# Kernel optimization log

Measured on AMD Instinct MI355X. Metric: run time of the kernel, lower is better.

Reference implementation:

```python
import jax, jax.numpy as jnp
import numpy as np

N_NODES = 100000


def gcn_conv(x, W, b, src, dst, n):
    # PyG GCNConv: add self-loops, symmetric deg^-1/2 normalization,
    # transform then gather/scatter-add aggregate.
    loop = jnp.arange(n, dtype=src.dtype)
    s = jnp.concatenate([src, loop])
    d = jnp.concatenate([dst, loop])
    deg = jax.ops.segment_sum(jnp.ones_like(d, dtype=x.dtype), d, num_segments=n)
    dinv = jnp.where(deg > 0, 1.0 / jnp.sqrt(deg), 0.0)
    norm = dinv[s] * dinv[d]                      # [E+N]
    h = x @ W                                     # [N, out]
    msgs = h[s] * norm[:, None]                   # gather + scale
    out = jax.ops.segment_sum(msgs, d, num_segments=n)  # scatter-add
    return out + b


def setup_inputs() -> dict:
    key = jax.random.key(0)
    k1, k2, k3, k4 = jax.random.split(key, 4)
    F_in, H, D = 128, 16, 128
    x = jax.random.normal(k1, (N_NODES, F_in), dtype=jnp.float32)
    edge_index = jax.random.randint(k2, (2, 1600000), 0, N_NODES, dtype=jnp.int64)
    W1 = jax.random.normal(k3, (F_in, H), dtype=jnp.float32) / np.sqrt(F_in)
    b1 = jnp.zeros((H,), dtype=jnp.float32)
    W2 = jax.random.normal(k4, (H, D), dtype=jnp.float32) / np.sqrt(H)
    b2 = jnp.zeros((D,), dtype=jnp.float32)
    return {"x": x, "edge_index": edge_index, "W1": W1, "b1": b1, "W2": W2, "b2": b2}


def reference(x, edge_index, W1, b1, W2, b2):
    src, dst = edge_index[0], edge_index[1]
    n = x.shape[0]
    h = jax.nn.relu(gcn_conv(x, W1, b1, src, dst, n))
    out = jax.nn.relu(gcn_conv(h, W2, b2, src, dst, n))
    return out
```

## Files before the change

### kernel.cpp

```cpp
#include <hip/hip_runtime.h>
#include <hip/hip_fp16.h>
#include <stdint.h>

#define F_IN  128
#define HID   16
#define F_OUT 128
#define NBK   512
#define NBLK  256
#define BCAP  4096

__device__ __forceinline__ int bucket_of(int d, int N) {
    return (int)(((long long)d * NBK) / N);
}
__device__ __forceinline__ int bucket_lo(int b, int N) {
    return (int)(((long long)b * N + NBK - 1) / NBK);
}

__global__ void k_partf(const int* __restrict__ ei, int* __restrict__ bcur,
                        uint32_t* __restrict__ pairs, int E, int N) {
    __shared__ int lh[NBK], lbase[NBK], lcur[NBK], lnlo[NBK];
    int blk = blockIdx.x, t = threadIdx.x;
    int C = (E + NBLK - 1) / NBLK;
    int e0 = blk * C;
    int e1 = e0 + C; if (e1 > E) e1 = E;
    for (int i = t; i < NBK; i += 256) { lh[i] = 0; lcur[i] = 0; lnlo[i] = bucket_lo(i, N); }
    __syncthreads();
    for (int e = e0 + t; e < e1; e += 256)
        atomicAdd(&lh[bucket_of(ei[E + e], N)], 1);
    __syncthreads();
    for (int w = 0; w < NBK; w += 256) {
        int i = (t + w + blk) & (NBK - 1);
        lbase[i] = i * BCAP + (lh[i] ? atomicAdd(&bcur[i], lh[i]) : 0);
    }
    __syncthreads();
    for (int e = e0 + t; e < e1; e += 256) {
        int s = ei[e];
        int d = ei[E + e];
        int b = bucket_of(d, N);
        int pos = lbase[b] + atomicAdd(&lcur[b], 1);
        if (pos < (b + 1) * BCAP)
            pairs[pos] = ((uint32_t)s << 10) | (uint32_t)(d - lnlo[b]);
    }
}

__global__ void __launch_bounds__(256) k_csr2(
        const uint32_t* __restrict__ pairs, const int* __restrict__ bcur,
        int* __restrict__ row_start, int* __restrict__ cnt,
        float* __restrict__ dinv, int* __restrict__ srcs, int N) {
    __shared__ int lcnt[256];
    __shared__ int loff[256];
    __shared__ int lcur[256];
    int b = blockIdx.x, t = threadIdx.x;
    int base = b * BCAP;
    int ec = bcur[b]; if (ec > BCAP) ec = BCAP;
    int nlo = bucket_lo(b, N);
    int nhi = bucket_lo(b + 1, N); if (nhi > N) nhi = N;
    int nn = nhi - nlo;
    lcnt[t] = 0;
    __syncthreads();
    for (int e = t; e < ec; e += 256)
        atomicAdd(&lcnt[pairs[base + e] & 1023u], 1);
    __syncthreads();
    int v = lcnt[t];
    int pv = (v + 3) & ~3;
    loff[t] = pv;
    __syncthreads();
    for (int o = 1; o < 256; o <<= 1) {
        int a = (t >= o) ? loff[t - o] : 0;
        __syncthreads();
        loff[t] += a;
        __syncthreads();
    }
    if (t < nn) {
        int gs = base + (loff[t] - pv);
        row_start[nlo + t] = gs;
        cnt[nlo + t]       = v;
        dinv[nlo + t]      = rsqrtf((float)(v + 1));
        lcur[t]            = gs;
    }
    __syncthreads();
    for (int e = t; e < ec; e += 256) {
        uint32_t p = pairs[base + e];
        int pos = atomicAdd(&lcur[p & 1023u], 1);
        srcs[pos] = (int)(p >> 10);
    }
}

#define XP1 132
__global__ void __launch_bounds__(256) k_transform1(
        const float* __restrict__ x, const float* __restrict__ W1,
        const float* __restrict__ dinv, __half* __restrict__ g1, int n) {
    __shared__ float sX[32 * XP1];
    __shared__ float sWt[HID * XP1];
    int t = threadIdx.x;
    int node0 = blockIdx.x * 32;
    for (int i = t; i < F_IN * HID; i += 256) {
        int k = i >> 4, f = i & 15;
        sWt[f * XP1 + k] = W1[i];
    }
    const float4* x4 = (const float4*)(x + (size_t)node0 * F_IN);
    int nrem = n - node0;
#pragma unroll
    for (int j = 0; j < 4; ++j) {
        int idx4 = t + j * 256;
        int nl = idx4 >> 5;
        int kk = (idx4 & 31) * 4;
        float4 v = make_float4(0.f, 0.f, 0.f, 0.f);
        if (nl < nrem) v = x4[idx4];
        *(float4*)&sX[nl * XP1 + kk] = v;
    }
    __syncthreads();
    int f  = t & 7;
    int nl = t >> 3;
    float a0 = 0.f, a1 = 0.f;
    const float* xr  = &sX[nl * XP1];
    const float* wr0 = &sWt[f * XP1];
    const float* wr1 = &sWt[(f + 8) * XP1];
#pragma unroll 4
    for (int k = 0; k < F_IN; k += 4) {
        float4 xv = *(const float4*)(xr + k);
        float4 w0 = *(const float4*)(wr0 + k);
        float4 w1 = *(const float4*)(wr1 + k);
        a0 += xv.x * w0.x + xv.y * w0.y + xv.z * w0.z + xv.w * w0.w;
        a1 += xv.x * w1.x + xv.y * w1.y + xv.z * w1.z + xv.w * w1.w;
    }
    int node = node0 + nl;
    if (node < n) {
        float di = dinv[node];
        g1[(size_t)node * HID + f]     = __float2half(di * a0);
        g1[(size_t)node * HID + f + 8] = __float2half(di * a1);
    }
}

__device__ __forceinline__ void add_h4(float* __restrict__ acc, const __half* __restrict__ ptr) {
    uint2 u = *(const uint2*)ptr;
    const __half2* h = (const __half2*)&u;
    float2 f0 = __half22float2(h[0]);
    float2 f1 = __half22float2(h[1]);
    acc[0] += f0.x; acc[1] += f0.y; acc[2] += f1.x; acc[3] += f1.y;
}

template<bool EP1>
__global__ void __launch_bounds__(256) k_gather_h(
        const __half* __restrict__ g, const int* __restrict__ srcs,
        const int* __restrict__ row_start, const int* __restrict__ cnt,
        const float* __restrict__ dinv, const float* __restrict__ b1,
        __half* __restrict__ outb, int n) {
    int t = blockIdx.x * blockDim.x + threadIdx.x;
    int node = t >> 2;
    int p = t & 3;
    if (node >= n) return;
    int rs  = row_start[node];
    int deg = cnt[node];
    float acc[4];
    {
        uint2 u = *(const uint2*)(g + (size_t)node * HID + p * 4);
        const __half2* h = (const __half2*)&u;
        float2 f0 = __half22float2(h[0]);
        float2 f1 = __half22float2(h[1]);
        acc[0] = f0.x; acc[1] = f0.y; acc[2] = f1.x; acc[3] = f1.y;
    }
    int j = 0;
    for (; j + 8 <= deg; j += 8) {
        int4 ia = *(const int4*)(srcs + rs + j);
        int4 ib = *(const int4*)(srcs + rs + j + 4);
        add_h4(acc, g + (size_t)ia.x * HID + p * 4);
        add_h4(acc, g + (size_t)ia.y * HID + p * 4);
        add_h4(acc, g + (size_t)ia.z * HID + p * 4);
        add_h4(acc, g + (size_t)ia.w * HID + p * 4);
        add_h4(acc, g + (size_t)ib.x * HID + p * 4);
        add_h4(acc, g + (size_t)ib.y * HID + p * 4);
        add_h4(acc, g + (size_t)ib.z * HID + p * 4);
        add_h4(acc, g + (size_t)ib.w * HID + p * 4);
    }
    if (j + 4 <= deg) {
        int4 ia = *(const int4*)(srcs + rs + j);
        add_h4(acc, g + (size_t)ia.x * HID + p * 4);
        add_h4(acc, g + (size_t)ia.y * HID + p * 4);
        add_h4(acc, g + (size_t)ia.z * HID + p * 4);
        add_h4(acc, g + (size_t)ia.w * HID + p * 4);
        j += 4;
    }
    for (; j < deg; ++j)
        add_h4(acc, g + (size_t)srcs[rs + j] * HID + p * 4);
    if (EP1) {
        float di = dinv[node];
#pragma unroll
        for (int i = 0; i < 4; ++i)
            acc[i] = di * fmaxf(di * acc[i] + b1[p * 4 + i], 0.0f);
    }
    uint2 o;
    __half2* oh = (__half2*)&o;
    oh[0] = __floats2half2_rn(acc[0], acc[1]);
    oh[1] = __floats2half2_rn(acc[2], acc[3]);
    *(uint2*)(outb + (size_t)node * HID + p * 4) = o;
}

__global__ void __launch_bounds__(256) k_transform2(
        const __half* __restrict__ agg, const float* __restrict__ W2,
        const float* __restrict__ b2, const float* __restrict__ dinv,
        float* __restrict__ out, int n) {
    int t = threadIdx.x;
    int d = t & 127;
    int h = t >> 7;
    int node0 = blockIdx.x * 32;
    float wcol[HID];
#pragma unroll
    for (int f = 0; f < HID; ++f) wcol[f] = W2[f * F_OUT + d];
    float bd = b2[d];
#pragma unroll 4
    for (int i = 0; i < 16; ++i) {
        int node = node0 + h + 2 * i;
        if (node >= n) continue;
        const uint4* av = (const uint4*)(agg + (size_t)node * HID);
        uint4 u0 = av[0], u1 = av[1];
        const __half2* h0 = (const __half2*)&u0;
        const __half2* h1 = (const __half2*)&u1;
        float s = 0.f;
#pragma unroll
        for (int q = 0; q < 4; ++q) {
            float2 f0 = __half22float2(h0[q]);
            float2 f1 = __half22float2(h1[q]);
            s += f0.x * wcol[2 * q]     + f0.y * wcol[2 * q + 1];
            s += f1.x * wcol[8 + 2 * q] + f1.y * wcol[9 + 2 * q];
        }
        out[(size_t)node * F_OUT + d] = fmaxf(dinv[node] * s + bd, 0.0f);
    }
}

extern "C" void kernel_launch(void* const* d_in, const int* in_sizes, int n_in,
                              void* d_out, int out_size, void* d_ws, size_t ws_size,
                              hipStream_t stream) {
    const float* x  = (const float*)d_in[0];
    const int*   ei = (const int*)d_in[1];
    const float* W1 = (const float*)d_in[2];
    const float* b1 = (const float*)d_in[3];
    const float* W2 = (const float*)d_in[4];
    const float* b2 = (const float*)d_in[5];
    float* out = (float*)d_out;

    const int N = in_sizes[0] / F_IN;
    const int E = in_sizes[1] / 2;

    float* dinv      = (float*)d_ws;
    int*   cnt       = (int*)(dinv + N);
    int*   row_start = cnt + N;
    int*   bcur      = row_start + N;
    int*   srcs      = bcur + NBK;
    uintptr_t xb = (uintptr_t)(srcs + (size_t)NBK * BCAP + 64);
    xb = (xb + 15) & ~(uintptr_t)15;
    uint32_t* pairs = (uint32_t*)xb;
    __half* bufA = (__half*)xb;
    __half* bufB = bufA + (size_t)N * HID;

    hipMemsetAsync(bcur, 0, NBK * sizeof(int), stream);
    k_partf<<<NBLK, 256, 0, stream>>>(ei, bcur, pairs, E, N);
    k_csr2 <<<NBK, 256, 0, stream>>>(pairs, bcur, row_start, cnt, dinv, srcs, N);

    k_transform1<<<(N + 31) / 32, 256, 0, stream>>>(x, W1, dinv, bufA, N);
    k_gather_h<true> <<<((size_t)N * 4 + 255) / 256, 256, 0, stream>>>(
        bufA, srcs, row_start, cnt, dinv, b1, bufB, N);
    k_gather_h<false><<<((size_t)N * 4 + 255) / 256, 256, 0, stream>>>(
        bufB, srcs, row_start, cnt, dinv, b1, bufA, N);
    k_transform2<<<(N + 31) / 32, 256, 0, stream>>>(bufA, W2, b2, dinv, out, N);
}
```

Before: 214.1 us.

## Stage partition writes in LDS by bucket and widen gather to 16-byte loads

The partition kernel now loads each block's edges into registers once and computes a local prefix scan over bucket counts. It scatters the packed pairs into shared memory sorted by bucket, then writes them to global memory in bucket-contiguous runs instead of scattered per-edge stores. The block count doubles so each block's chunk (about 3125 edges) fits the fixed per-thread register and LDS buffers. Separately, the gather kernels use 2 threads per node with 16-byte half loads instead of 4 threads with 8-byte loads. This halves the thread count but leaves fewer threads in flight to hide gather latency. Edges beyond EPT*256 per block would be silently dropped if E changed.

```diff
diff --git a/kernel.cpp b/kernel.cpp
--- a/kernel.cpp
+++ b/kernel.cpp
@@ -6,8 +6,10 @@
 #define HID   16
 #define F_OUT 128
 #define NBK   512
-#define NBLK  256
+#define NBLK  512
 #define BCAP  4096
+#define CHUNK_MAX 4096
+#define EPT   16
 
 __device__ __forceinline__ int bucket_of(int d, int N) {
     return (int)(((long long)d * NBK) / N);
@@ -16,30 +18,79 @@
     return (int)(((long long)b * N + NBK - 1) / NBK);
 }
 
-__global__ void k_partf(const int* __restrict__ ei, int* __restrict__ bcur,
-                        uint32_t* __restrict__ pairs, int E, int N) {
-    __shared__ int lh[NBK], lbase[NBK], lcur[NBK], lnlo[NBK];
+__global__ void __launch_bounds__(256) k_partf(
+        const int* __restrict__ ei, int* __restrict__ bcur,
+        uint32_t* __restrict__ pairs, int E, int N) {
+    __shared__ int lh[NBK];
+    __shared__ int lofs[NBK];
+    __shared__ int lcur[NBK];
+    __shared__ int gbase[NBK];
+    __shared__ int lnlo[NBK];
+    __shared__ int loff[256];
+    __shared__ uint32_t spairs[CHUNK_MAX];
+    __shared__ uint16_t sbkt[CHUNK_MAX];
+
     int blk = blockIdx.x, t = threadIdx.x;
     int C = (E + NBLK - 1) / NBLK;
     int e0 = blk * C;
     int e1 = e0 + C; if (e1 > E) e1 = E;
-    for (int i = t; i < NBK; i += 256) { lh[i] = 0; lcur[i] = 0; lnlo[i] = bucket_lo(i, N); }
-    __syncthreads();
-    for (int e = e0 + t; e < e1; e += 256)
-        atomicAdd(&lh[bucket_of(ei[E + e], N)], 1);
-    __syncthreads();
+    int ecnt = e1 - e0;
+
+    for (int i = t; i < NBK; i += 256) { lh[i] = 0; lnlo[i] = bucket_lo(i, N); }
+    __syncthreads();
+
+    int es[EPT], ed[EPT], eb[EPT];
+#pragma unroll
+    for (int k = 0; k < EPT; ++k) {
+        int e = e0 + k * 256 + t;
+        if (e < e1) {
+            es[k] = ei[e];
+            ed[k] = ei[E + e];
+            eb[k] = bucket_of(ed[k], N);
+            atomicAdd(&lh[eb[k]], 1);
+        } else eb[k] = -1;
+    }
+    __syncthreads();
+
+    int a0 = lh[2 * t], a1 = lh[2 * t + 1];
+    int s2 = a0 + a1;
+    loff[t] = s2;
+    __syncthreads();
+    for (int o = 1; o < 256; o <<= 1) {
+        int a = (t >= o) ? loff[t - o] : 0;
+        __syncthreads();
+        loff[t] += a;
+        __syncthreads();
+    }
+    int excl = loff[t] - s2;
+    lofs[2 * t]     = excl;
+    lofs[2 * t + 1] = excl + a0;
+    lcur[2 * t]     = excl;
+    lcur[2 * t + 1] = excl + a0;
+    __syncthreads();
+
     for (int w = 0; w < NBK; w += 256) {
         int i = (t + w + blk) & (NBK - 1);
-        lbase[i] = i * BCAP + (lh[i] ? atomicAdd(&bcur[i], lh[i]) : 0);
-    }
-    __syncthreads();
-    for (int e = e0 + t; e < e1; e += 256) {
-        int s = ei[e];
-        int d = ei[E + e];
-        int b = bucket_of(d, N);
-        int pos = lbase[b] + atomicAdd(&lcur[b], 1);
-        if (pos < (b + 1) * BCAP)
-            pairs[pos] = ((uint32_t)s << 10) | (uint32_t)(d - lnlo[b]);
+        int h = lh[i];
+        gbase[i] = h ? atomicAdd(&bcur[i], h) : 0;
+    }
+
+#pragma unroll
+    for (int k = 0; k < EPT; ++k) {
+        if (eb[k] >= 0) {
+            int b = eb[k];
+            int idx = atomicAdd(&lcur[b], 1);
+            spairs[idx] = ((uint32_t)es[k] << 10) | (uint32_t)(ed[k] - lnlo[b]);
+            sbkt[idx]   = (uint16_t)b;
+        }
+    }
+    __syncthreads();
+
+    for (int i = t; i < ecnt; i += 256) {
+        int b = sbkt[i];
+        int pos = gbase[b] + (i - lofs[b]);
+        if (pos < BCAP)
+            pairs[(size_t)b * BCAP + pos] = spairs[i];
     }
 }
 
@@ -132,12 +183,15 @@
     }
 }
 
-__device__ __forceinline__ void add_h4(float* __restrict__ acc, const __half* __restrict__ ptr) {
-    uint2 u = *(const uint2*)ptr;
+__device__ __forceinline__ void add_h8(float* __restrict__ acc, const __half* __restrict__ ptr) {
+    uint4 u = *(const uint4*)ptr;
     const __half2* h = (const __half2*)&u;
-    float2 f0 = __half22float2(h[0]);
-    float2 f1 = __half22float2(h[1]);
-    acc[0] += f0.x; acc[1] += f0.y; acc[2] += f1.x; acc[3] += f1.y;
+#pragma unroll
+    for (int q = 0; q < 4; ++q) {
+        float2 f = __half22float2(h[q]);
+        acc[2 * q]     += f.x;
+        acc[2 * q + 1] += f.y;
+    }
 }
 
 template<bool EP1>
@@ -147,53 +201,56 @@
         const float* __restrict__ dinv, const float* __restrict__ b1,
         __half* __restrict__ outb, int n) {
     int t = blockIdx.x * blockDim.x + threadIdx.x;
-    int node = t >> 2;
-    int p = t & 3;
+    int node = t >> 1;
+    int p = t & 1;
     if (node >= n) return;
     int rs  = row_start[node];
     int deg = cnt[node];
-    float acc[4];
+    float acc[8];
     {
-        uint2 u = *(const uint2*)(g + (size_t)node * HID + p * 4);
+        uint4 u = *(const uint4*)(g + (size_t)node * HID + p * 8);
         const __half2* h = (const __half2*)&u;
-        float2 f0 = __half22float2(h[0]);
-        float2 f1 = __half22float2(h[1]);
-        acc[0] = f0.x; acc[1] = f0.y; acc[2] = f1.x; acc[3] = f1.y;
+#pragma unroll
+        for (int q = 0; q < 4; ++q) {
+            float2 f = __half22float2(h[q]);
+            acc[2 * q] = f.x; acc[2 * q + 1] = f.y;
+        }
     }
     int j = 0;
     for (; j + 8 <= deg; j += 8) {
         int4 ia = *(const int4*)(srcs + rs + j);
         int4 ib = *(const int4*)(srcs + rs + j + 4);
-        add_h4(acc, g + (size_t)ia.x * HID + p * 4);
-        add_h4(acc, g + (size_t)ia.y * HID + p * 4);
-        add_h4(acc, g + (size_t)ia.z * HID + p * 4);
-        add_h4(acc, g + (size_t)ia.w * HID + p * 4);
-        add_h4(acc, g + (size_t)ib.x * HID + p * 4);
-        add_h4(acc, g + (size_t)ib.y * HID + p * 4);
-        add_h4(acc, g + (size_t)ib.z * HID + p * 4);
-        add_h4(acc, g + (size_t)ib.w * HID + p * 4);
+        add_h8(acc, g + (size_t)ia.x * HID + p * 8);
+        add_h8(acc, g + (size_t)ia.y * HID + p * 8);
+        add_h8(acc, g + (size_t)ia.z * HID + p * 8);
+        add_h8(acc, g + (size_t)ia.w * HID + p * 8);
+        add_h8(acc, g + (size_t)ib.x * HID + p * 8);
+        add_h8(acc, g + (size_t)ib.y * HID + p * 8);
+        add_h8(acc, g + (size_t)ib.z * HID + p * 8);
+        add_h8(acc, g + (size_t)ib.w * HID + p * 8);
     }
     if (j + 4 <= deg) {
         int4 ia = *(const int4*)(srcs + rs + j);
-        add_h4(acc, g + (size_t)ia.x * HID + p * 4);
-        add_h4(acc, g + (size_t)ia.y * HID + p * 4);
-        add_h4(acc, g + (size_t)ia.z * HID + p * 4);
-        add_h4(acc, g + (size_t)ia.w * HID + p * 4);
+        add_h8(acc, g + (size_t)ia.x * HID + p * 8);
+        add_h8(acc, g + (size_t)ia.y * HID + p * 8);
+        add_h8(acc, g + (size_t)ia.z * HID + p * 8);
+        add_h8(acc, g + (size_t)ia.w * HID + p * 8);
         j += 4;
     }
     for (; j < deg; ++j)
-        add_h4(acc, g + (size_t)srcs[rs + j] * HID + p * 4);
+        add_h8(acc, g + (size_t)srcs[rs + j] * HID + p * 8);
     if (EP1) {
         float di = dinv[node];
 #pragma unroll
-        for (int i = 0; i < 4; ++i)
-            acc[i] = di * fmaxf(di * acc[i] + b1[p * 4 + i], 0.0f);
-    }
-    uint2 o;
+        for (int i = 0; i < 8; ++i)
+            acc[i] = di * fmaxf(di * acc[i] + b1[p * 8 + i], 0.0f);
+    }
+    uint4 o;
     __half2* oh = (__half2*)&o;
-    oh[0] = __floats2half2_rn(acc[0], acc[1]);
-    oh[1] = __floats2half2_rn(acc[2], acc[3]);
-    *(uint2*)(outb + (size_t)node * HID + p * 4) = o;
+#pragma unroll
+    for (int q = 0; q < 4; ++q)
+        oh[q] = __floats2half2_rn(acc[2 * q], acc[2 * q + 1]);
+    *(uint4*)(outb + (size_t)node * HID + p * 8) = o;
 }
 
 __global__ void __launch_bounds__(256) k_transform2(
@@ -258,9 +315,9 @@
     k_csr2 <<<NBK, 256, 0, stream>>>(pairs, bcur, row_start, cnt, dinv, srcs, N);
 
     k_transform1<<<(N + 31) / 32, 256, 0, stream>>>(x, W1, dinv, bufA, N);
-    k_gather_h<true> <<<((size_t)N * 4 + 255) / 256, 256, 0, stream>>>(
+    k_gather_h<true> <<<((size_t)N * 2 + 255) / 256, 256, 0, stream>>>(
         bufA, srcs, row_start, cnt, dinv, b1, bufB, N);
-    k_gather_h<false><<<((size_t)N * 4 + 255) / 256, 256, 0, stream>>>(
+    k_gather_h<false><<<((size_t)N * 2 + 255) / 256, 256, 0, stream>>>(
         bufB, srcs, row_start, cnt, dinv, b1, bufA, N);
     k_transform2<<<(N + 31) / 32, 256, 0, stream>>>(bufA, W2, b2, dinv, out, N);
 }
```

New measurement: 211.0 us. No clear change (-1.4%).
